# Performance work log

Measured on AMD Instinct MI355X. Metric: run time of the kernel, lower is better.

## Reference

```python
import jax, jax.numpy as jnp
import numpy as np

B, L, D, H, C = 16, 512, 1280, 512, 5


def setup_inputs() -> dict:
    key = jax.random.key(0)
    ks = jax.random.split(key, 20)
    emb = jax.random.normal(ks[0], (B, L, D), jnp.float32)
    lengths = jax.random.randint(ks[1], (B,), 16, L + 1)
    attention_mask = (jnp.arange(L)[None, :] < lengths[:, None]).astype(jnp.int32)
    sc = 1.0 / np.sqrt(H)
    u = lambda k, s: jax.random.uniform(k, s, jnp.float32, -sc, sc)
    return dict(
        embeddings=emb,
        attention_mask=attention_mask,
        h0=jax.random.normal(ks[2], (2, B, H), jnp.float32),
        c0=jax.random.normal(ks[3], (2, B, H), jnp.float32),
        w_ih_f=u(ks[4], (4 * H, D)), w_hh_f=u(ks[5], (4 * H, H)),
        b_ih_f=u(ks[6], (4 * H,)), b_hh_f=u(ks[7], (4 * H,)),
        w_ih_b=u(ks[8], (4 * H, D)), w_hh_b=u(ks[9], (4 * H, H)),
        b_ih_b=u(ks[10], (4 * H,)), b_hh_b=u(ks[11], (4 * H,)),
        w_out=u(ks[12], (2 * H, C)), b_out=u(ks[13], (C,)),
        crf_start=jax.random.normal(ks[14], (C,), jnp.float32) * 0.1,
        crf_end=jax.random.normal(ks[15], (C,), jnp.float32) * 0.1,
        crf_trans=jax.random.normal(ks[16], (C, C), jnp.float32) * 0.1,
    )


def _lstm_dir(x, h0, c0, w_ih, w_hh, b_ih, b_hh):
    # x: [B, T, D] -> hidden states [B, T, H]; PyTorch gate order (i, f, g, o)
    xg = jnp.einsum('btd,gd->btg', x, w_ih) + b_ih + b_hh  # [B, T, 4H]

    def step(carry, xw_t):
        h, c = carry
        g = xw_t + h @ w_hh.T
        i, f, gg, o = jnp.split(g, 4, axis=-1)
        c = jax.nn.sigmoid(f) * c + jax.nn.sigmoid(i) * jnp.tanh(gg)
        h = jax.nn.sigmoid(o) * jnp.tanh(c)
        return (h, c), h

    _, hs = jax.lax.scan(step, (h0, c0), xg.transpose(1, 0, 2))
    return hs.transpose(1, 0, 2)


def _emissions(embeddings, attention_mask, h0, c0, w_ih_f, w_hh_f, b_ih_f, b_hh_f,
               w_ih_b, w_hh_b, b_ih_b, b_hh_b, w_out, b_out):
    lengths = attention_mask.sum(axis=1)
    x = embeddings[:, 1:-1]                                   # drop CLS position, shift left
    Tp = x.shape[1]
    valid = jnp.arange(Tp)[None, :] < (lengths - 2)[:, None]  # remove_cls crop [1:len-1], left-aligned pad
    x = jnp.where(valid[:, :, None], x, 0.0)
    hf = _lstm_dir(x, h0[0], c0[0], w_ih_f, w_hh_f, b_ih_f, b_hh_f)
    hb = _lstm_dir(x[:, ::-1], h0[1], c0[1], w_ih_b, w_hh_b, b_ih_b, b_hh_b)[:, ::-1]
    h = jnp.concatenate([hf, hb], axis=-1)                    # [B, Tp, 2H]
    return h @ w_out + b_out, valid


def _viterbi_decode(emissions, mask, start, end, trans):
    Bn, Tp, Ct = emissions.shape
    ident = jnp.arange(Ct, dtype=jnp.int32)
    score0 = start[None, :] + emissions[:, 0]                 # [B, C]

    def step(score, inp):
        emit_t, m_t = inp                                      # [B, C], [B]
        br = score[:, :, None] + trans[None] + emit_t[:, None, :]
        ns = br.max(axis=1)
        idx = br.argmax(axis=1).astype(jnp.int32)
        idx = jnp.where(m_t[:, None], idx, ident[None, :])     # identity backpointer past seq end
        score = jnp.where(m_t[:, None], ns, score)
        return score, idx

    score, hist = jax.lax.scan(step, score0,
                               (emissions[:, 1:].transpose(1, 0, 2), mask[:, 1:].T))
    score = score + end[None, :]
    last = jnp.argmax(score, axis=-1).astype(jnp.int32)        # [B]
    bidx = jnp.arange(Bn)

    def bstep(tag, idx_t):
        prev = idx_t[bidx, tag]
        return prev, prev

    _, prevs = jax.lax.scan(bstep, last, hist, reverse=True)   # [Tp-1, B]
    tags = jnp.concatenate([prevs, last[None, :]], axis=0).transpose(1, 0)
    return tags


def reference(embeddings, attention_mask, h0, c0, w_ih_f, w_hh_f, b_ih_f, b_hh_f,
              w_ih_b, w_hh_b, b_ih_b, b_hh_b, w_out, b_out, crf_start, crf_end, crf_trans):
    emissions, valid = _emissions(embeddings, attention_mask, h0, c0,
                                  w_ih_f, w_hh_f, b_ih_f, b_hh_f,
                                  w_ih_b, w_hh_b, b_ih_b, b_hh_b, w_out, b_out)
    tags = _viterbi_decode(emissions, valid, crf_start, crf_end, crf_trans)
    return tags, valid  # tags valid where mask True (past-end entries repeat last tag)
```

## Files before the change

kernel.cpp:

```cpp
#include <hip/hip_runtime.h>

typedef unsigned short u16;
typedef unsigned int u32;
typedef __bf16 bf16x8 __attribute__((ext_vector_type(8)));
typedef u16 u16x8 __attribute__((ext_vector_type(8)));
typedef float f32x4 __attribute__((ext_vector_type(4)));

#define B_ 16
#define T_ 510
#define H_ 512
#define N_ 4096
#define KSPLIT 2560

#define OFF_ABIG  0ull
#define OFF_BBIG  41943040ull
#define OFF_BIAS  62914560ull
#define OFF_XG    62930944ull
#define OFF_HS    197148672ull
#define OFF_EMIS  230572032ull
#define OFF_V     230735232ull
#define OFF_FLAGS 230735296ull
#define OFF_HBUF  230735552ull
#define OFF_HBUFB  (OFF_EMIS)
#define OFF_FLAGSB (OFF_EMIS + 131072ull)
#define OFF_PROBE  (OFF_EMIS + 131328ull)
#define OFF_CTRL   (OFF_EMIS + 131584ull)

#define MAGIC_ 0x5EC0FFEE
#define POLL_BUDGET 65536
#define ARB_BUDGET  262144

#define GL_LDS(g, s) __builtin_amdgcn_global_load_lds(                      \
    (const __attribute__((address_space(1))) void*)(g),                     \
    (__attribute__((address_space(3))) void*)(s), 16, 0, 0)

__device__ __forceinline__ u16 f2bf(float x) {
  u32 u = __float_as_uint(x);
  u32 r = (u + 0x7fffu + ((u >> 16) & 1u)) >> 16;
  return (u16)r;
}
__device__ __forceinline__ float bf2f(u16 h) { return __uint_as_float(((u32)h) << 16); }

__device__ __forceinline__ int ld_cc(const int* p) {
  int f;
  asm volatile("global_load_dword %0, %1, off sc0 sc1\n\ts_waitcnt vmcnt(0)" : "=v"(f) : "v"(p) : "memory");
  return f;
}
__device__ __forceinline__ void st_cc(int* p, int v) {
  asm volatile("global_store_dword %0, %1, off sc0 sc1\n\ts_waitcnt vmcnt(0)" :: "v"(p), "v"(v) : "memory");
}
__device__ __forceinline__ void st_plain(int* p, int v) {
  asm volatile("global_store_dword %0, %1, off\n\ts_waitcnt vmcnt(0)" :: "v"(p), "v"(v) : "memory");
}

__global__ __launch_bounds__(256) void k_prep(const int* __restrict__ mask, int* __restrict__ V,
                                              int* __restrict__ flagsA, int* __restrict__ flagsB,
                                              int* __restrict__ probe, int* __restrict__ ctrl) {
  __shared__ int red[4];
  int b = blockIdx.x, tid = threadIdx.x;
  int s = mask[b * 512 + tid] + mask[b * 512 + 256 + tid];
  for (int off = 32; off; off >>= 1) s += __shfl_down(s, off);
  if ((tid & 63) == 0) red[tid >> 6] = s;
  __syncthreads();
  if (tid == 0) V[b] = red[0] + red[1] + red[2] + red[3] - 2;
  if (b == 0 && tid < 64) flagsA[tid] = 0;
  if (b == 2 && tid < 64) flagsB[tid] = 0;
  if (b == 3 && tid < 64) probe[tid] = 0;
  if (b == 1 && tid < 16) ctrl[tid] = 0;
}

__global__ __launch_bounds__(256) void k_valid(const int* __restrict__ V, int* __restrict__ out) {
  int idx = blockIdx.x * 256 + threadIdx.x;
  if (idx < B_ * T_) {
    int b = idx / T_, t = idx - b * T_;
    out[B_ * T_ + idx] = (t < V[b]) ? 1 : 0;
  }
}

__global__ __launch_bounds__(320) void k_splitA(const float* __restrict__ emb, const int* __restrict__ V,
                                                u16* __restrict__ Abig) {
  int row = blockIdx.x;
  int k0 = threadIdx.x * 4;
  u16* dst = Abig + (size_t)row * KSPLIT;
  float4 v = {0.f, 0.f, 0.f, 0.f};
  if (row < B_ * T_) {
    int b = row / T_, t = row - b * T_;
    if (t < V[b]) v = *(const float4*)(emb + (size_t)(b * 512 + t + 1) * 1280 + k0);
  }
  float vs[4] = {v.x, v.y, v.z, v.w};
  ushort4 hi, lo;
  u16 h0_ = f2bf(vs[0]); u16 l0_ = f2bf(vs[0] - bf2f(h0_));
  u16 h1_ = f2bf(vs[1]); u16 l1_ = f2bf(vs[1] - bf2f(h1_));
  u16 h2_ = f2bf(vs[2]); u16 l2_ = f2bf(vs[2] - bf2f(h2_));
  u16 h3_ = f2bf(vs[3]); u16 l3_ = f2bf(vs[3] - bf2f(h3_));
  hi.x = h0_; hi.y = h1_; hi.z = h2_; hi.w = h3_;
  lo.x = l0_; lo.y = l1_; lo.z = l2_; lo.w = l3_;
  *(ushort4*)(dst + k0) = hi;
  *(ushort4*)(dst + 1280 + k0) = lo;
}

__global__ __launch_bounds__(320) void k_splitB(const float* __restrict__ wf, const float* __restrict__ wb,
                                                const float* __restrict__ bihf, const float* __restrict__ bhhf,
                                                const float* __restrict__ bihb, const float* __restrict__ bhhb,
                                                u16* __restrict__ Bbig, float* __restrict__ bias) {
  int n = blockIdx.x;
  int k0 = threadIdx.x * 4;
  int d = n >> 11, g = n & 2047;
  const float* w = (d ? wb : wf) + (size_t)g * 1280;
  float4 v = *(const float4*)(w + k0);
  float vs[4] = {v.x, v.y, v.z, v.w};
  ushort4 hi, lo;
  u16 h0_ = f2bf(vs[0]); u16 l0_ = f2bf(vs[0] - bf2f(h0_));
  u16 h1_ = f2bf(vs[1]); u16 l1_ = f2bf(vs[1] - bf2f(h1_));
  u16 h2_ = f2bf(vs[2]); u16 l2_ = f2bf(vs[2] - bf2f(h2_));
  u16 h3_ = f2bf(vs[3]); u16 l3_ = f2bf(vs[3] - bf2f(h3_));
  hi.x = h0_; hi.y = h1_; hi.z = h2_; hi.w = h3_;
  lo.x = l0_; lo.y = l1_; lo.z = l2_; lo.w = l3_;
  u16* dst = Bbig + (size_t)n * KSPLIT;
  *(ushort4*)(dst + k0) = hi;
  *(ushort4*)(dst + 1280 + k0) = lo;
  if (threadIdx.x == 0) bias[n] = d ? (bihb[g] + bhhb[g]) : (bihf[g] + bhhf[g]);
}

__global__ __launch_bounds__(256, 2) void k_gemm(const u16* __restrict__ A, const u16* __restrict__ Bt,
                                                 const float* __restrict__ bias, float* __restrict__ C) {
  __shared__ __align__(16) u16 As[128 * 64];
  __shared__ __align__(16) u16 Bs[128 * 64];
  const int tid = threadIdx.x;
  const int w = tid >> 6, l = tid & 63;
  const int wm = w >> 1, wn = w & 1;
  const int bm = blockIdx.x, bn = blockIdx.y;
  f32x4 acc[4][4];
#pragma unroll
  for (int m = 0; m < 4; ++m)
#pragma unroll
    for (int n = 0; n < 4; ++n) acc[m][n] = (f32x4){0.f, 0.f, 0.f, 0.f};

  const int rQ = tid >> 3;
  const int cB = (tid & 7) * 16;
  const char* gA = (const char*)(A + (size_t)(bm * 128) * KSPLIT) + cB;
  const char* gB = (const char*)(Bt + (size_t)(bn * 128) * KSPLIT) + cB;

  for (int kt = 0; kt < 60; ++kt) {
    const int s = kt / 20, ks = kt - s * 20;
    const int aOff = ((s == 2) ? 1280 : 0) + ks * 64;
    const int bOff = ((s == 1) ? 1280 : 0) + ks * 64;
    __syncthreads();
#pragma unroll
    for (int q = 0; q < 4; ++q) {
      GL_LDS(gA + ((size_t)(q * 32 + rQ) * KSPLIT + aOff) * 2, (char*)As + q * 4096 + tid * 16);
      GL_LDS(gB + ((size_t)(q * 32 + rQ) * KSPLIT + bOff) * 2, (char*)Bs + q * 4096 + tid * 16);
    }
    __syncthreads();
#pragma unroll
    for (int kc = 0; kc < 2; ++kc) {
      bf16x8 af[4], bfr[4];
      const int kByte = kc * 64 + (l >> 4) * 16;
#pragma unroll
      for (int m = 0; m < 4; ++m)
        af[m] = *(const bf16x8*)((const char*)As + (wm * 64 + m * 16 + (l & 15)) * 128 + kByte);
#pragma unroll
      for (int n = 0; n < 4; ++n)
        bfr[n] = *(const bf16x8*)((const char*)Bs + (wn * 64 + n * 16 + (l & 15)) * 128 + kByte);
#pragma unroll
      for (int m = 0; m < 4; ++m)
#pragma unroll
        for (int n = 0; n < 4; ++n)
          acc[m][n] = __builtin_amdgcn_mfma_f32_16x16x32_bf16(af[m], bfr[n], acc[m][n], 0, 0, 0);
    }
  }
#pragma unroll
  for (int n = 0; n < 4; ++n) {
    const int gc = bn * 128 + wn * 64 + n * 16 + (l & 15);
    const float bv = bias[gc];
#pragma unroll
    for (int m = 0; m < 4; ++m) {
      const int gr0 = bm * 128 + wm * 64 + m * 16 + (l >> 4) * 4;
#pragma unroll
      for (int r = 0; r < 4; ++r) C[(size_t)(gr0 + r) * N_ + gc] = acc[m][n][r] + bv;
    }
  }
}

template <int COH>
__device__ void run_recur(int dir, int sub, const float* __restrict__ xg, const float* __restrict__ whh,
                          const float* __restrict__ h0, const float* __restrict__ c0,
                          float* __restrict__ hs, u16* __restrict__ hbuf, int* __restrict__ flags,
                          u16* lds_a, float* epil, float* hsh) {
  const int tid = threadIdx.x;
  const int w = tid >> 6, l = tid & 63;
  const int c = l & 15, kg = l >> 4;
  const int gate = c >> 2, uloc = c & 3;
  const int ug = sub * 16 + w * 4 + uloc;
  constexpr int GB = COH ? 9 : 0;

  __syncthreads();

  bf16x8 whi[16], wlo[16];
  {
    const float* wrow = whh + (size_t)(gate * 512 + ug) * 512 + kg * 8;
#pragma unroll
    for (int kc = 0; kc < 16; ++kc) {
      float4 v0 = *(const float4*)(wrow + kc * 32);
      float4 v1 = *(const float4*)(wrow + kc * 32 + 4);
      float vs[8] = {v0.x, v0.y, v0.z, v0.w, v1.x, v1.y, v1.z, v1.w};
      u16x8 hi, lo;
#pragma unroll
      for (int j = 0; j < 8; ++j) {
        u16 h = f2bf(vs[j]);
        hi[j] = h;
        lo[j] = f2bf(vs[j] - bf2f(h));
      }
      whi[kc] = __builtin_bit_cast(bf16x8, hi);
      wlo[kc] = __builtin_bit_cast(bf16x8, lo);
    }
  }

  const int eb = l & 15, eu = l >> 4;
  const int eug = sub * 16 + w * 4 + eu;
  float creg = c0[(dir * 16 + eb) * 512 + eug];
  {
    float h = h0[(dir * 16 + eb) * 512 + eug];
    u16 hh = f2bf(h), hl = f2bf(h - bf2f(hh));
    size_t base = (size_t)(dir * 2) * 8192;
    u16* p0 = hbuf + base + eb * 512 + eug;
    u16* p1 = hbuf + base + 8192 + eb * 512 + eug;
    if constexpr (COH) {
      asm volatile("global_store_short %0, %1, off\n\tglobal_store_short %2, %3, off\n\ts_waitcnt vmcnt(0)"
                   :: "v"(p0), "v"((u32)hh), "v"(p1), "v"((u32)hl) : "memory");
    } else {
      asm volatile("global_store_short %0, %1, off sc0 sc1\n\tglobal_store_short %2, %3, off sc0 sc1\n\ts_waitcnt vmcnt(0)"
                   :: "v"(p0), "v"((u32)hh), "v"(p1), "v"((u32)hl) : "memory");
    }
  }
  __syncthreads();
  if (tid == 0) {
    if constexpr (COH) st_plain(flags + dir * 32 + sub, 1 + GB);
    else st_cc(flags + dir * 32 + sub, 1 + GB);
  }

  for (int t = 0; t < T_; ++t) {
    const int trow = dir ? (T_ - 1 - t) : t;
    f32x4 acc0;
    {
      const int n = dir * 2048 + gate * 512 + ug;
#pragma unroll
      for (int r = 0; r < 4; ++r) acc0[r] = xg[(size_t)((kg * 4 + r) * T_ + trow) * N_ + n];
    }
    if (w == 0) {
      const int* fp = flags + (dir << 5) + (l & 31);
      while (true) {
        int f;
        asm volatile("global_load_dword %0, %1, off sc0 sc1\n\ts_waitcnt vmcnt(0)" : "=v"(f) : "v"(fp) : "memory");
        if (__all(f >= t + 1 + GB)) break;
        if constexpr (!COH) __builtin_amdgcn_s_sleep(1);
      }
    }
    __syncthreads();

    {
      const u16* src = hbuf + (size_t)(((t & 1) * 2 + dir) * 2) * 8192;
      uint4 v[8];
#pragma unroll
      for (int q = 0; q < 8; ++q) {
        const char* p = (const char*)src + q * 4096 + tid * 16;
        asm volatile("global_load_dwordx4 %0, %1, off sc0 sc1" : "=v"(v[q]) : "v"(p) : "memory");
      }
      asm volatile("s_waitcnt vmcnt(0)" ::: "memory");
      __builtin_amdgcn_sched_barrier(0);
#pragma unroll
      for (int q = 0; q < 8; ++q) {
        int off = q * 4096 + tid * 16;
        int var = off >> 14;
        int rem = off & 16383;
        int b = rem >> 10;
        int inrow = rem & 1023;
        *(uint4*)((char*)lds_a + var * 16384 + b * 1024 + (inrow ^ ((b & 7) << 4))) = v[q];
      }
    }
    __syncthreads();

    f32x4 acc1 = (f32x4){0.f, 0.f, 0.f, 0.f};
    f32x4 acc2 = (f32x4){0.f, 0.f, 0.f, 0.f};
    f32x4 acc3 = (f32x4){0.f, 0.f, 0.f, 0.f};
    f32x4 acc4 = (f32x4){0.f, 0.f, 0.f, 0.f};
    f32x4 acc5 = (f32x4){0.f, 0.f, 0.f, 0.f};
#pragma unroll
    for (int kc = 0; kc < 16; ++kc) {
      const int rowb = l & 15;
      const int koff = (kc * 64 + kg * 16) ^ ((rowb & 7) << 4);
      bf16x8 ahi = *(const bf16x8*)((const char*)lds_a + rowb * 1024 + koff);
      bf16x8 alo = *(const bf16x8*)((const char*)lds_a + 16384 + rowb * 1024 + koff);
      if (kc & 1) {
        acc3 = __builtin_amdgcn_mfma_f32_16x16x32_bf16(ahi, whi[kc], acc3, 0, 0, 0);
        acc4 = __builtin_amdgcn_mfma_f32_16x16x32_bf16(ahi, wlo[kc], acc4, 0, 0, 0);
        acc5 = __builtin_amdgcn_mfma_f32_16x16x32_bf16(alo, whi[kc], acc5, 0, 0, 0);
      } else {
        acc0 = __builtin_amdgcn_mfma_f32_16x16x32_bf16(ahi, whi[kc], acc0, 0, 0, 0);
        acc1 = __builtin_amdgcn_mfma_f32_16x16x32_bf16(ahi, wlo[kc], acc1, 0, 0, 0);
        acc2 = __builtin_amdgcn_mfma_f32_16x16x32_bf16(alo, whi[kc], acc2, 0, 0, 0);
      }
    }
    f32x4 acc = ((acc0 + acc3) + (acc1 + acc4)) + (acc2 + acc5);

#pragma unroll
    for (int r = 0; r < 4; ++r) epil[(w * 16 + kg * 4 + r) * 17 + c] = acc[r];
    asm volatile("s_waitcnt lgkmcnt(0)" ::: "memory");
    __builtin_amdgcn_sched_barrier(0);
    const float gi = epil[(w * 16 + eb) * 17 + 0 + eu];
    const float gf = epil[(w * 16 + eb) * 17 + 4 + eu];
    const float gg = epil[(w * 16 + eb) * 17 + 8 + eu];
    const float go = epil[(w * 16 + eb) * 17 + 12 + eu];
    const float si = 1.f / (1.f + __expf(-gi));
    const float sf = 1.f / (1.f + __expf(-gf));
    const float so = 1.f / (1.f + __expf(-go));
    const float tg = tanhf(gg);
    creg = sf * creg + si * tg;
    const float h = so * tanhf(creg);
    hsh[eb * 17 + w * 4 + eu] = h;
    __syncthreads();
    const int sb = tid >> 4, su = tid & 15;
    const float hv = hsh[sb * 17 + su];
    {
      u16 hh = f2bf(hv), hl = f2bf(hv - bf2f(hh));
      size_t base = (size_t)((((t + 1) & 1) * 2 + dir) * 2) * 8192;
      u16* p0 = hbuf + base + sb * 512 + sub * 16 + su;
      if constexpr (COH) {
        asm volatile("global_store_short %0, %1, off\n\tglobal_store_short %2, %3, off\n\ts_waitcnt vmcnt(0)"
                     :: "v"(p0), "v"((u32)hh), "v"(p0 + 8192), "v"((u32)hl) : "memory");
      } else {
        asm volatile("global_store_short %0, %1, off sc0 sc1\n\tglobal_store_short %2, %3, off sc0 sc1\n\ts_waitcnt vmcnt(0)"
                     :: "v"(p0), "v"((u32)hh), "v"(p0 + 8192), "v"((u32)hl) : "memory");
      }
    }
    __syncthreads();
    if (tid == 0) {
      if constexpr (COH) st_plain(flags + dir * 32 + sub, t + 2 + GB);
      else st_cc(flags + dir * 32 + sub, t + 2 + GB);
    }
    hs[(size_t)((dir * 16 + sb) * T_ + trow) * 512 + sub * 16 + su] = hv;
  }
}

__global__ __launch_bounds__(256, 1) void k_recur(const float* __restrict__ xg, const float* __restrict__ whh_f,
                                                  const float* __restrict__ whh_b, const float* __restrict__ h0,
                                                  const float* __restrict__ c0, float* __restrict__ hs,
                                                  u16* __restrict__ hbufA, u16* __restrict__ hbufB,
                                                  int* __restrict__ flagsA, int* __restrict__ flagsB,
                                                  int* __restrict__ probe, int* __restrict__ ctrl) {
  __shared__ __align__(16) u16 lds_a[16384];
  __shared__ float epil[4 * 16 * 17];
  __shared__ float hsh[16 * 17];
  __shared__ int s_act, s_cfg;

  const int tid = threadIdx.x;

  if (tid == 0) {
    int xcc;
    asm volatile("s_getreg_b32 %0, hwreg(HW_REG_XCC_ID)" : "=s"(xcc));
    xcc &= 7;
    int slot = 99;
    if (xcc < 2) slot = __hip_atomic_fetch_add(&ctrl[4 + xcc], 1, __ATOMIC_RELAXED, __HIP_MEMORY_SCOPE_AGENT);
    const int roleA = (xcc < 2 && slot < 32);
    const int dir = xcc, sub = slot;

    if (roleA) {
      int mg = MAGIC_;
      asm volatile("global_store_dword %0, %1, off\n\ts_waitcnt vmcnt(0)" :: "v"(probe + dir * 32 + sub), "v"(mg) : "memory");
      st_cc(flagsA + dir * 32 + sub, 2);
      bool complete = false;
      for (int it = 0; it < POLL_BUDGET && !complete; ++it) {
        complete = true;
        for (int j = 0; j < 32; ++j)
          if (ld_cc(flagsA + dir * 32 + j) < 2) { complete = false; break; }
        if (!complete) __builtin_amdgcn_s_sleep(16);
      }
      int myval = 99;
      if (complete) {
        bool ok = true;
        for (int j = 0; j < 32; ++j)
          if (ld_cc(probe + dir * 32 + j) != MAGIC_) { ok = false; break; }
        if (ok) myval = 3;
      }
      st_cc(flagsA + dir * 32 + sub, myval);
      if (sub == 0) {
        bool go = false;
        for (int it = 0; it < POLL_BUDGET; ++it) {
          int n3 = 0; bool bad = false;
          for (int j = 0; j < 32; ++j) {
            int f = ld_cc(flagsA + dir * 32 + j);
            if (f == 99) { bad = true; break; }
            if (f == 3) ++n3;
          }
          if (bad) break;
          if (n3 == 32) { go = true; break; }
          __builtin_amdgcn_s_sleep(16);
        }
        st_cc(&ctrl[12 + dir], go ? 1 : 2);
      }
    }

    if (blockIdx.x == 0) {
      int v0 = 0, v1 = 0;
      for (int it = 0; it < ARB_BUDGET; ++it) {
        v0 = ld_cc(&ctrl[12]);
        v1 = ld_cc(&ctrl[13]);
        if (v0 && v1) break;
        __builtin_amdgcn_s_sleep(16);
      }
      st_cc(&ctrl[14], 4 | (v0 == 1 ? 1 : 0) | (v1 == 1 ? 2 : 0));
    }

    int cfg;
    do {
      cfg = ld_cc(&ctrl[14]);
      if (!cfg) __builtin_amdgcn_s_sleep(16);
    } while (!cfg);

    s_cfg = cfg;
    s_act = (roleA && (cfg & (1 << dir))) ? (dir | (sub << 1)) : -1;
  }
  __syncthreads();
  const int act = s_act, cfg = s_cfg;

  if (act >= 0) {
    const int adir = act & 1, asub = act >> 1;
    run_recur<1>(adir, asub, xg, adir ? whh_b : whh_f, h0, c0, hs, hbufA, flagsA, lds_a, epil, hsh);
  }
  if (blockIdx.x < 64) {
    const int mdir = (int)blockIdx.x >> 5, msub = (int)blockIdx.x & 31;
    if (!(cfg & (1 << mdir)))
      run_recur<0>(mdir, msub, xg, mdir ? whh_b : whh_f, h0, c0, hs, hbufB, flagsB, lds_a, epil, hsh);
  }
}

__global__ __launch_bounds__(256) void k_emis(const float* __restrict__ hs, const float* __restrict__ wout,
                                              const float* __restrict__ bout, float* __restrict__ e) {
  const int tid = threadIdx.x;
  const int w = tid >> 6, l = tid & 63;
  const int row = blockIdx.x * 4 + w;
  const int b = row / T_, t = row - b * T_;
  const float* hf = hs + (size_t)(b * T_ + t) * 512;
  const float* hb = hs + (size_t)((16 + b) * T_ + t) * 512;
  float a0 = 0, a1 = 0, a2 = 0, a3 = 0, a4 = 0;
#pragma unroll
  for (int it = 0; it < 8; ++it) {
    int u = it * 64 + l;
    float hv = hf[u];
    const float* wr = wout + u * 5;
    a0 += hv * wr[0]; a1 += hv * wr[1]; a2 += hv * wr[2]; a3 += hv * wr[3]; a4 += hv * wr[4];
  }
#pragma unroll
  for (int it = 0; it < 8; ++it) {
    int u = it * 64 + l;
    float hv = hb[u];
    const float* wr = wout + (512 + u) * 5;
    a0 += hv * wr[0]; a1 += hv * wr[1]; a2 += hv * wr[2]; a3 += hv * wr[3]; a4 += hv * wr[4];
  }
  for (int off = 32; off; off >>= 1) {
    a0 += __shfl_down(a0, off);
    a1 += __shfl_down(a1, off);
    a2 += __shfl_down(a2, off);
    a3 += __shfl_down(a3, off);
    a4 += __shfl_down(a4, off);
  }
  if (l == 0) {
    float* ep = e + (size_t)row * 5;
    ep[0] = a0 + bout[0];
    ep[1] = a1 + bout[1];
    ep[2] = a2 + bout[2];
    ep[3] = a3 + bout[3];
    ep[4] = a4 + bout[4];
  }
}

__global__ __launch_bounds__(64) void k_viterbi(const float* __restrict__ e, const int* __restrict__ V,
                                                const float* __restrict__ start, const float* __restrict__ endv,
                                                const float* __restrict__ trans, int* __restrict__ out) {
  __shared__ float els[T_ * 5];
  __shared__ unsigned char hist[(T_ - 1) * 5];
  __shared__ float strans[25];
  const int b = blockIdx.x, l = threadIdx.x;
  for (int i = l; i < T_ * 5; i += 64) els[i] = e[(size_t)b * T_ * 5 + i];
  if (l < 25) strans[l] = trans[l];
  const int Vb = V[b];
  __syncthreads();
  const int cl = (l < 5) ? l : 0;
  float score = (l < 5) ? (start[l] + els[l]) : -1e30f;
  for (int t = 1; t < T_; ++t) {
    const bool valid = t < Vb;
    float m = -1e30f;
    int arg = 0;
#pragma unroll
    for (int p = 0; p < 5; ++p) {
      float v = __shfl(score, p) + strans[p * 5 + cl];
      if (v > m) { m = v; arg = p; }
    }
    if (l < 5) {
      if (valid) {
        score = m + els[t * 5 + l];
        hist[(t - 1) * 5 + l] = (unsigned char)arg;
      } else {
        hist[(t - 1) * 5 + l] = (unsigned char)l;
      }
    }
  }
  float sc = (l < 5) ? (score + endv[l]) : -1e30f;
  int last = 0;
  float mb = -1e30f;
#pragma unroll
  for (int p = 0; p < 5; ++p) {
    float v = __shfl(sc, p);
    if (v > mb) { mb = v; last = p; }
  }
  __syncthreads();
  if (l == 0) {
    int tag = last;
    out[b * T_ + (T_ - 1)] = tag;
    for (int t = T_ - 2; t >= 0; --t) {
      tag = hist[t * 5 + tag];
      out[b * T_ + t] = tag;
    }
  }
}

extern "C" void kernel_launch(void* const* d_in, const int* in_sizes, int n_in, void* d_out, int out_size,
                              void* d_ws, size_t ws_size, hipStream_t stream) {
  const float* emb = (const float*)d_in[0];
  const int* amask = (const int*)d_in[1];
  const float* h0 = (const float*)d_in[2];
  const float* c0 = (const float*)d_in[3];
  const float* wihf = (const float*)d_in[4];
  const float* whhf = (const float*)d_in[5];
  const float* bihf = (const float*)d_in[6];
  const float* bhhf = (const float*)d_in[7];
  const float* wihb = (const float*)d_in[8];
  const float* whhb = (const float*)d_in[9];
  const float* bihb = (const float*)d_in[10];
  const float* bhhb = (const float*)d_in[11];
  const float* wout = (const float*)d_in[12];
  const float* bout = (const float*)d_in[13];
  const float* cstart = (const float*)d_in[14];
  const float* cend = (const float*)d_in[15];
  const float* ctrans = (const float*)d_in[16];

  char* ws = (char*)d_ws;
  u16* Abig = (u16*)(ws + OFF_ABIG);
  u16* Bbig = (u16*)(ws + OFF_BBIG);
  float* bias = (float*)(ws + OFF_BIAS);
  float* xg = (float*)(ws + OFF_XG);
  float* hs = (float*)(ws + OFF_HS);
  float* emis = (float*)(ws + OFF_EMIS);
  int* V = (int*)(ws + OFF_V);
  int* flagsA = (int*)(ws + OFF_FLAGS);
  u16* hbufA = (u16*)(ws + OFF_HBUF);
  u16* hbufB = (u16*)(ws + OFF_HBUFB);
  int* flagsB = (int*)(ws + OFF_FLAGSB);
  int* probe = (int*)(ws + OFF_PROBE);
  int* ctrl = (int*)(ws + OFF_CTRL);
  int* out = (int*)d_out;

  hipLaunchKernelGGL(k_prep, dim3(16), dim3(256), 0, stream, amask, V, flagsA, flagsB, probe, ctrl);
  hipLaunchKernelGGL(k_valid, dim3(32), dim3(256), 0, stream, V, out);
  hipLaunchKernelGGL(k_splitA, dim3(8192), dim3(320), 0, stream, emb, V, Abig);
  hipLaunchKernelGGL(k_splitB, dim3(4096), dim3(320), 0, stream, wihf, wihb, bihf, bhhf, bihb, bhhb, Bbig, bias);
  hipLaunchKernelGGL(k_gemm, dim3(64, 32), dim3(256), 0, stream, Abig, Bbig, bias, xg);
  hipLaunchKernelGGL(k_recur, dim3(256), dim3(256), 0, stream, xg, whhf, whhb, h0, c0, hs, hbufA, hbufB,
                     flagsA, flagsB, probe, ctrl);
  hipLaunchKernelGGL(k_emis, dim3(2040), dim3(256), 0, stream, hs, wout, bout, emis);
  hipLaunchKernelGGL(k_viterbi, dim3(16), dim3(64), 0, stream, emis, V, cstart, cend, ctrans, out);
}
```

Before: 1.775 ms.

## Replace per-step flag polling with generation-tagged hidden-state chunks in LSTM recurrence

The recurrent kernel no longer publishes h through a separate buffer plus a per-block flag. Each block now writes 16-byte chunks that carry the bf16 hi/lo h values together with a generation counter, and consumers spin on the chunk tags directly. This removes the flag store/poll round trip and a barrier from every serial timestep. It also issues the xg input loads early so they overlap the wait, and replaces tanhf/division with exp+rcp approximations. The chunk buffers are placed at workspace offset 0 (the Abig region), which depends on Abig being dead by then, and rcp-based activations are slightly less accurate.

```diff
diff --git a/kernel.cpp b/kernel.cpp
--- a/kernel.cpp
+++ b/kernel.cpp
@@ -5,6 +5,8 @@
 typedef __bf16 bf16x8 __attribute__((ext_vector_type(8)));
 typedef u16 u16x8 __attribute__((ext_vector_type(8)));
 typedef float f32x4 __attribute__((ext_vector_type(4)));
+typedef u32 u32x2 __attribute__((ext_vector_type(2)));
+typedef u32 u32x4 __attribute__((ext_vector_type(4)));
 
 #define B_ 16
 #define T_ 510
@@ -20,11 +22,10 @@
 #define OFF_EMIS  230572032ull
 #define OFF_V     230735232ull
 #define OFF_FLAGS 230735296ull
-#define OFF_HBUF  230735552ull
-#define OFF_HBUFB  (OFF_EMIS)
-#define OFF_FLAGSB (OFF_EMIS + 131072ull)
 #define OFF_PROBE  (OFF_EMIS + 131328ull)
 #define OFF_CTRL   (OFF_EMIS + 131584ull)
+#define CHUNKA_OFF 0ull
+#define CHUNKB_OFF 262144ull
 
 #define MAGIC_ 0x5EC0FFEE
 #define POLL_BUDGET 65536
@@ -49,13 +50,19 @@
 __device__ __forceinline__ void st_cc(int* p, int v) {
   asm volatile("global_store_dword %0, %1, off sc0 sc1\n\ts_waitcnt vmcnt(0)" :: "v"(p), "v"(v) : "memory");
 }
-__device__ __forceinline__ void st_plain(int* p, int v) {
-  asm volatile("global_store_dword %0, %1, off\n\ts_waitcnt vmcnt(0)" :: "v"(p), "v"(v) : "memory");
+
+__device__ __forceinline__ float sigm_f(float x) {
+  float e = __expf(-x);
+  return __builtin_amdgcn_rcpf(1.f + e);
+}
+__device__ __forceinline__ float tanh_f(float x) {
+  float e = __expf(2.f * x);
+  return 1.f - 2.f * __builtin_amdgcn_rcpf(e + 1.f);
 }
 
 __global__ __launch_bounds__(256) void k_prep(const int* __restrict__ mask, int* __restrict__ V,
-                                              int* __restrict__ flagsA, int* __restrict__ flagsB,
-                                              int* __restrict__ probe, int* __restrict__ ctrl) {
+                                              int* __restrict__ flagsA, int* __restrict__ probe,
+                                              int* __restrict__ ctrl) {
   __shared__ int red[4];
   int b = blockIdx.x, tid = threadIdx.x;
   int s = mask[b * 512 + tid] + mask[b * 512 + 256 + tid];
@@ -64,9 +71,14 @@
   __syncthreads();
   if (tid == 0) V[b] = red[0] + red[1] + red[2] + red[3] - 2;
   if (b == 0 && tid < 64) flagsA[tid] = 0;
-  if (b == 2 && tid < 64) flagsB[tid] = 0;
   if (b == 3 && tid < 64) probe[tid] = 0;
   if (b == 1 && tid < 16) ctrl[tid] = 0;
+}
+
+__global__ __launch_bounds__(256) void k_zero(char* __restrict__ p) {
+  u32x4 z = (u32x4){0u, 0u, 0u, 0u};
+  char* dst = p + ((size_t)blockIdx.x * 256 + threadIdx.x) * 16;
+  asm volatile("global_store_dwordx4 %0, %1, off sc0 sc1" :: "v"(dst), "v"(z) : "memory");
 }
 
 __global__ __launch_bounds__(256) void k_valid(const int* __restrict__ V, int* __restrict__ out) {
@@ -183,16 +195,31 @@
 }
 
 template <int COH>
+__device__ __forceinline__ void emit_chunks(char* buf, int sub, u32 gen, const u16* pack) {
+  const int tid = threadIdx.x;
+  if (tid < 128) {
+    const int sb = tid >> 3, r = tid & 7, p = r >> 2, j = r & 3;
+    const u32* pw = (const u32*)(pack + p * 256 + sb * 16 + j * 4);
+    u32x4 val;
+    val[0] = pw[0]; val[1] = pw[1]; val[2] = gen; val[3] = 0u;
+    char* dst = buf + sb * 4096 + p * 2048 + (sub * 4 + j) * 16;
+    if constexpr (COH)
+      asm volatile("global_store_dwordx4 %0, %1, off" :: "v"(dst), "v"(val) : "memory");
+    else
+      asm volatile("global_store_dwordx4 %0, %1, off sc0 sc1" :: "v"(dst), "v"(val) : "memory");
+  }
+}
+
+template <int COH>
 __device__ void run_recur(int dir, int sub, const float* __restrict__ xg, const float* __restrict__ whh,
                           const float* __restrict__ h0, const float* __restrict__ c0,
-                          float* __restrict__ hs, u16* __restrict__ hbuf, int* __restrict__ flags,
-                          u16* lds_a, float* epil, float* hsh) {
+                          float* __restrict__ hs, char* __restrict__ cb,
+                          u16* lds_a, float* epil, u16* pack) {
   const int tid = threadIdx.x;
   const int w = tid >> 6, l = tid & 63;
   const int c = l & 15, kg = l >> 4;
   const int gate = c >> 2, uloc = c & 3;
   const int ug = sub * 16 + w * 4 + uloc;
-  constexpr int GB = COH ? 9 : 0;
 
   __syncthreads();
 
@@ -216,75 +243,61 @@
     }
   }
 
-  const int eb = l & 15, eu = l >> 4;
-  const int eug = sub * 16 + w * 4 + eu;
-  float creg = c0[(dir * 16 + eb) * 512 + eug];
+  const int sb = tid >> 4, su = tid & 15;
+  const int gu = sub * 16 + su;
+  float creg = c0[(dir * 16 + sb) * 512 + gu];
   {
-    float h = h0[(dir * 16 + eb) * 512 + eug];
+    float h = h0[(dir * 16 + sb) * 512 + gu];
     u16 hh = f2bf(h), hl = f2bf(h - bf2f(hh));
-    size_t base = (size_t)(dir * 2) * 8192;
-    u16* p0 = hbuf + base + eb * 512 + eug;
-    u16* p1 = hbuf + base + 8192 + eb * 512 + eug;
-    if constexpr (COH) {
-      asm volatile("global_store_short %0, %1, off\n\tglobal_store_short %2, %3, off\n\ts_waitcnt vmcnt(0)"
-                   :: "v"(p0), "v"((u32)hh), "v"(p1), "v"((u32)hl) : "memory");
-    } else {
-      asm volatile("global_store_short %0, %1, off sc0 sc1\n\tglobal_store_short %2, %3, off sc0 sc1\n\ts_waitcnt vmcnt(0)"
-                   :: "v"(p0), "v"((u32)hh), "v"(p1), "v"((u32)hl) : "memory");
-    }
+    pack[sb * 16 + su] = hh;
+    pack[256 + sb * 16 + su] = hl;
   }
   __syncthreads();
-  if (tid == 0) {
-    if constexpr (COH) st_plain(flags + dir * 32 + sub, 1 + GB);
-    else st_cc(flags + dir * 32 + sub, 1 + GB);
-  }
+  emit_chunks<COH>(cb + 65536, sub, 1u, pack);
 
   for (int t = 0; t < T_; ++t) {
     const int trow = dir ? (T_ - 1 - t) : t;
-    f32x4 acc0;
-    {
-      const int n = dir * 2048 + gate * 512 + ug;
-#pragma unroll
-      for (int r = 0; r < 4; ++r) acc0[r] = xg[(size_t)((kg * 4 + r) * T_ + trow) * N_ + n];
-    }
-    if (w == 0) {
-      const int* fp = flags + (dir << 5) + (l & 31);
-      while (true) {
-        int f;
-        asm volatile("global_load_dword %0, %1, off sc0 sc1\n\ts_waitcnt vmcnt(0)" : "=v"(f) : "v"(fp) : "memory");
-        if (__all(f >= t + 1 + GB)) break;
-        if constexpr (!COH) __builtin_amdgcn_s_sleep(1);
-      }
-    }
-    __syncthreads();
-
-    {
-      const u16* src = hbuf + (size_t)(((t & 1) * 2 + dir) * 2) * 8192;
-      uint4 v[8];
-#pragma unroll
-      for (int q = 0; q < 8; ++q) {
-        const char* p = (const char*)src + q * 4096 + tid * 16;
-        asm volatile("global_load_dwordx4 %0, %1, off sc0 sc1" : "=v"(v[q]) : "v"(p) : "memory");
-      }
+    const u32 gen = (u32)(t + 1);
+    const char* sbuf = cb + ((t + 1) & 1) * 65536;
+
+    u32x4 v[16];
+#pragma unroll
+    for (int i = 0; i < 16; ++i) {
+      const char* p = sbuf + ((size_t)(tid + 256 * i)) * 16;
+      asm volatile("global_load_dwordx4 %0, %1, off sc0 sc1" : "=v"(v[i]) : "v"(p) : "memory");
+    }
+    float xv[4];
+#pragma unroll
+    for (int g = 0; g < 4; ++g) {
+      const float* p = xg + (size_t)(sb * T_ + trow) * N_ + dir * 2048 + g * 512 + gu;
+      asm volatile("global_load_dword %0, %1, off" : "=v"(xv[g]) : "v"(p) : "memory");
+    }
+    asm volatile("s_waitcnt vmcnt(4)" ::: "memory");
+    __builtin_amdgcn_sched_barrier(0);
+    while (true) {
+      u32 bad = 0;
+#pragma unroll
+      for (int i = 0; i < 16; ++i) bad |= (v[i][2] != gen) ? (1u << i) : 0u;
+      if (!bad) break;
+#pragma unroll
+      for (int i = 0; i < 16; ++i)
+        if (bad & (1u << i)) {
+          const char* p = sbuf + ((size_t)(tid + 256 * i)) * 16;
+          asm volatile("global_load_dwordx4 %0, %1, off sc0 sc1" : "=v"(v[i]) : "v"(p) : "memory");
+        }
       asm volatile("s_waitcnt vmcnt(0)" ::: "memory");
       __builtin_amdgcn_sched_barrier(0);
-#pragma unroll
-      for (int q = 0; q < 8; ++q) {
-        int off = q * 4096 + tid * 16;
-        int var = off >> 14;
-        int rem = off & 16383;
-        int b = rem >> 10;
-        int inrow = rem & 1023;
-        *(uint4*)((char*)lds_a + var * 16384 + b * 1024 + (inrow ^ ((b & 7) << 4))) = v[q];
-      }
+    }
+#pragma unroll
+    for (int i = 0; i < 16; ++i) {
+      int ci = tid + 256 * i;
+      int b = ci >> 8, pl = (ci >> 7) & 1, k = ci & 127;
+      int off = pl * 16384 + b * 1024 + ((k * 8) ^ ((b & 7) << 4));
+      *(u32x2*)((char*)lds_a + off) = (u32x2){v[i][0], v[i][1]};
     }
     __syncthreads();
 
-    f32x4 acc1 = (f32x4){0.f, 0.f, 0.f, 0.f};
-    f32x4 acc2 = (f32x4){0.f, 0.f, 0.f, 0.f};
-    f32x4 acc3 = (f32x4){0.f, 0.f, 0.f, 0.f};
-    f32x4 acc4 = (f32x4){0.f, 0.f, 0.f, 0.f};
-    f32x4 acc5 = (f32x4){0.f, 0.f, 0.f, 0.f};
+    f32x4 a0 = (f32x4){0.f, 0.f, 0.f, 0.f}, a1 = a0, a2 = a0, a3 = a0, a4 = a0, a5 = a0;
 #pragma unroll
     for (int kc = 0; kc < 16; ++kc) {
       const int rowb = l & 15;
@@ -292,65 +305,53 @@
       bf16x8 ahi = *(const bf16x8*)((const char*)lds_a + rowb * 1024 + koff);
       bf16x8 alo = *(const bf16x8*)((const char*)lds_a + 16384 + rowb * 1024 + koff);
       if (kc & 1) {
-        acc3 = __builtin_amdgcn_mfma_f32_16x16x32_bf16(ahi, whi[kc], acc3, 0, 0, 0);
-        acc4 = __builtin_amdgcn_mfma_f32_16x16x32_bf16(ahi, wlo[kc], acc4, 0, 0, 0);
-        acc5 = __builtin_amdgcn_mfma_f32_16x16x32_bf16(alo, whi[kc], acc5, 0, 0, 0);
+        a3 = __builtin_amdgcn_mfma_f32_16x16x32_bf16(ahi, whi[kc], a3, 0, 0, 0);
+        a4 = __builtin_amdgcn_mfma_f32_16x16x32_bf16(ahi, wlo[kc], a4, 0, 0, 0);
+        a5 = __builtin_amdgcn_mfma_f32_16x16x32_bf16(alo, whi[kc], a5, 0, 0, 0);
       } else {
-        acc0 = __builtin_amdgcn_mfma_f32_16x16x32_bf16(ahi, whi[kc], acc0, 0, 0, 0);
-        acc1 = __builtin_amdgcn_mfma_f32_16x16x32_bf16(ahi, wlo[kc], acc1, 0, 0, 0);
-        acc2 = __builtin_amdgcn_mfma_f32_16x16x32_bf16(alo, whi[kc], acc2, 0, 0, 0);
-      }
-    }
-    f32x4 acc = ((acc0 + acc3) + (acc1 + acc4)) + (acc2 + acc5);
-
-#pragma unroll
-    for (int r = 0; r < 4; ++r) epil[(w * 16 + kg * 4 + r) * 17 + c] = acc[r];
-    asm volatile("s_waitcnt lgkmcnt(0)" ::: "memory");
+        a0 = __builtin_amdgcn_mfma_f32_16x16x32_bf16(ahi, whi[kc], a0, 0, 0, 0);
+        a1 = __builtin_amdgcn_mfma_f32_16x16x32_bf16(ahi, wlo[kc], a1, 0, 0, 0);
+        a2 = __builtin_amdgcn_mfma_f32_16x16x32_bf16(alo, whi[kc], a2, 0, 0, 0);
+      }
+    }
+    f32x4 acc = ((a0 + a3) + (a1 + a4)) + (a2 + a5);
+
+#pragma unroll
+    for (int r = 0; r < 4; ++r) epil[w * 280 + (kg * 4 + r) * 17 + c] = acc[r];
+    __syncthreads();
+    asm volatile("s_waitcnt vmcnt(0)" ::: "memory");
     __builtin_amdgcn_sched_barrier(0);
-    const float gi = epil[(w * 16 + eb) * 17 + 0 + eu];
-    const float gf = epil[(w * 16 + eb) * 17 + 4 + eu];
-    const float gg = epil[(w * 16 + eb) * 17 + 8 + eu];
-    const float go = epil[(w * 16 + eb) * 17 + 12 + eu];
-    const float si = 1.f / (1.f + __expf(-gi));
-    const float sf = 1.f / (1.f + __expf(-gf));
-    const float so = 1.f / (1.f + __expf(-go));
-    const float tg = tanhf(gg);
+    const int ew = su >> 2, ec = su & 3;
+    const float gi = epil[ew * 280 + sb * 17 + 0 + ec] + xv[0];
+    const float gf = epil[ew * 280 + sb * 17 + 4 + ec] + xv[1];
+    const float gg = epil[ew * 280 + sb * 17 + 8 + ec] + xv[2];
+    const float go = epil[ew * 280 + sb * 17 + 12 + ec] + xv[3];
+    const float si = sigm_f(gi);
+    const float sf = sigm_f(gf);
+    const float so = sigm_f(go);
+    const float tg = tanh_f(gg);
     creg = sf * creg + si * tg;
-    const float h = so * tanhf(creg);
-    hsh[eb * 17 + w * 4 + eu] = h;
+    const float h = so * tanh_f(creg);
+    {
+      u16 hh = f2bf(h), hl = f2bf(h - bf2f(hh));
+      pack[sb * 16 + su] = hh;
+      pack[256 + sb * 16 + su] = hl;
+    }
     __syncthreads();
-    const int sb = tid >> 4, su = tid & 15;
-    const float hv = hsh[sb * 17 + su];
-    {
-      u16 hh = f2bf(hv), hl = f2bf(hv - bf2f(hh));
-      size_t base = (size_t)((((t + 1) & 1) * 2 + dir) * 2) * 8192;
-      u16* p0 = hbuf + base + sb * 512 + sub * 16 + su;
-      if constexpr (COH) {
-        asm volatile("global_store_short %0, %1, off\n\tglobal_store_short %2, %3, off\n\ts_waitcnt vmcnt(0)"
-                     :: "v"(p0), "v"((u32)hh), "v"(p0 + 8192), "v"((u32)hl) : "memory");
-      } else {
-        asm volatile("global_store_short %0, %1, off sc0 sc1\n\tglobal_store_short %2, %3, off sc0 sc1\n\ts_waitcnt vmcnt(0)"
-                     :: "v"(p0), "v"((u32)hh), "v"(p0 + 8192), "v"((u32)hl) : "memory");
-      }
-    }
-    __syncthreads();
-    if (tid == 0) {
-      if constexpr (COH) st_plain(flags + dir * 32 + sub, t + 2 + GB);
-      else st_cc(flags + dir * 32 + sub, t + 2 + GB);
-    }
-    hs[(size_t)((dir * 16 + sb) * T_ + trow) * 512 + sub * 16 + su] = hv;
+    emit_chunks<COH>(cb + (t & 1) * 65536, sub, (u32)(t + 2), pack);
+    hs[(size_t)((dir * 16 + sb) * T_ + trow) * 512 + gu] = h;
   }
 }
 
 __global__ __launch_bounds__(256, 1) void k_recur(const float* __restrict__ xg, const float* __restrict__ whh_f,
                                                   const float* __restrict__ whh_b, const float* __restrict__ h0,
                                                   const float* __restrict__ c0, float* __restrict__ hs,
-                                                  u16* __restrict__ hbufA, u16* __restrict__ hbufB,
-                                                  int* __restrict__ flagsA, int* __restrict__ flagsB,
-                                                  int* __restrict__ probe, int* __restrict__ ctrl) {
+                                                  char* __restrict__ chunkA, char* __restrict__ chunkB,
+                                                  int* __restrict__ flagsA, int* __restrict__ probe,
+                                                  int* __restrict__ ctrl) {
   __shared__ __align__(16) u16 lds_a[16384];
-  __shared__ float epil[4 * 16 * 17];
-  __shared__ float hsh[16 * 17];
+  __shared__ float epil[4 * 280];
+  __shared__ u16 pack[512];
   __shared__ int s_act, s_cfg;
 
   const int tid = threadIdx.x;
@@ -425,12 +426,14 @@
 
   if (act >= 0) {
     const int adir = act & 1, asub = act >> 1;
-    run_recur<1>(adir, asub, xg, adir ? whh_b : whh_f, h0, c0, hs, hbufA, flagsA, lds_a, epil, hsh);
+    run_recur<1>(adir, asub, xg, adir ? whh_b : whh_f, h0, c0, hs,
+                 chunkA + adir * 131072, lds_a, epil, pack);
   }
   if (blockIdx.x < 64) {
     const int mdir = (int)blockIdx.x >> 5, msub = (int)blockIdx.x & 31;
     if (!(cfg & (1 << mdir)))
-      run_recur<0>(mdir, msub, xg, mdir ? whh_b : whh_f, h0, c0, hs, hbufB, flagsB, lds_a, epil, hsh);
+      run_recur<0>(mdir, msub, xg, mdir ? whh_b : whh_f, h0, c0, hs,
+                   chunkB + mdir * 131072, lds_a, epil, pack);
   }
 }
 
@@ -553,20 +556,20 @@
   float* emis = (float*)(ws + OFF_EMIS);
   int* V = (int*)(ws + OFF_V);
   int* flagsA = (int*)(ws + OFF_FLAGS);
-  u16* hbufA = (u16*)(ws + OFF_HBUF);
-  u16* hbufB = (u16*)(ws + OFF_HBUFB);
-  int* flagsB = (int*)(ws + OFF_FLAGSB);
   int* probe = (int*)(ws + OFF_PROBE);
   int* ctrl = (int*)(ws + OFF_CTRL);
+  char* chunkA = ws + CHUNKA_OFF;
+  char* chunkB = ws + CHUNKB_OFF;
   int* out = (int*)d_out;
 
-  hipLaunchKernelGGL(k_prep, dim3(16), dim3(256), 0, stream, amask, V, flagsA, flagsB, probe, ctrl);
+  hipLaunchKernelGGL(k_prep, dim3(16), dim3(256), 0, stream, amask, V, flagsA, probe, ctrl);
   hipLaunchKernelGGL(k_valid, dim3(32), dim3(256), 0, stream, V, out);
   hipLaunchKernelGGL(k_splitA, dim3(8192), dim3(320), 0, stream, emb, V, Abig);
   hipLaunchKernelGGL(k_splitB, dim3(4096), dim3(320), 0, stream, wihf, wihb, bihf, bhhf, bihb, bhhb, Bbig, bias);
   hipLaunchKernelGGL(k_gemm, dim3(64, 32), dim3(256), 0, stream, Abig, Bbig, bias, xg);
-  hipLaunchKernelGGL(k_recur, dim3(256), dim3(256), 0, stream, xg, whhf, whhb, h0, c0, hs, hbufA, hbufB,
-                     flagsA, flagsB, probe, ctrl);
+  hipLaunchKernelGGL(k_zero, dim3(128), dim3(256), 0, stream, chunkA);
+  hipLaunchKernelGGL(k_recur, dim3(256), dim3(256), 0, stream, xg, whhf, whhb, h0, c0, hs,
+                     chunkA, chunkB, flagsA, probe, ctrl);
   hipLaunchKernelGGL(k_emis, dim3(2040), dim3(256), 0, stream, hs, wout, bout, emis);
   hipLaunchKernelGGL(k_viterbi, dim3(16), dim3(64), 0, stream, emis, V, cstart, cend, ctrans, out);
 }
```

Result: slower. 1.826 ms (+2.9%).

## Add runtime probe to use sc0-only loads for same-XCC recurrence handshakes

Applied to the files above, without the earlier changes.

Extends the startup handshake among the 32 blocks of each direction. If they can verify that stores are seen through the shared L2 using loads without the sc1 system-coherence bit, they switch to a third recurrence mode. In that mode flag polling and h-buffer loads use sc0 only, with an occasional full-coherence flag load as a fallback. The aim is to cut the latency of the per-timestep cross-block synchronisation. The cost is a longer multi-phase handshake at startup and a risk of stale reads if the probe's verdict is wrong.

```diff
diff --git a/kernel.cpp b/kernel.cpp
--- a/kernel.cpp
+++ b/kernel.cpp
@@ -5,6 +5,7 @@
 typedef __bf16 bf16x8 __attribute__((ext_vector_type(8)));
 typedef u16 u16x8 __attribute__((ext_vector_type(8)));
 typedef float f32x4 __attribute__((ext_vector_type(4)));
+typedef u32 u32x4 __attribute__((ext_vector_type(4)));
 
 #define B_ 16
 #define T_ 510
@@ -25,9 +26,13 @@
 #define OFF_FLAGSB (OFF_EMIS + 131072ull)
 #define OFF_PROBE  (OFF_EMIS + 131328ull)
 #define OFF_CTRL   (OFF_EMIS + 131584ull)
-
-#define MAGIC_ 0x5EC0FFEE
+#define OFF_PROBE2 (OFF_EMIS + 131648ull)
+
+#define MAGIC_  0x5EC0FFEE
+#define MAGIC2_ 0x7A57C0DE
+#define MAGIC3_ 0x3C0DE777
 #define POLL_BUDGET 65536
+#define PHB_BUDGET  8192
 #define ARB_BUDGET  262144
 
 #define GL_LDS(g, s) __builtin_amdgcn_global_load_lds(                      \
@@ -46,6 +51,11 @@
   asm volatile("global_load_dword %0, %1, off sc0 sc1\n\ts_waitcnt vmcnt(0)" : "=v"(f) : "v"(p) : "memory");
   return f;
 }
+__device__ __forceinline__ int ld_se(const int* p) {
+  int f;
+  asm volatile("global_load_dword %0, %1, off sc0\n\ts_waitcnt vmcnt(0)" : "=v"(f) : "v"(p) : "memory");
+  return f;
+}
 __device__ __forceinline__ void st_cc(int* p, int v) {
   asm volatile("global_store_dword %0, %1, off sc0 sc1\n\ts_waitcnt vmcnt(0)" :: "v"(p), "v"(v) : "memory");
 }
@@ -55,7 +65,8 @@
 
 __global__ __launch_bounds__(256) void k_prep(const int* __restrict__ mask, int* __restrict__ V,
                                               int* __restrict__ flagsA, int* __restrict__ flagsB,
-                                              int* __restrict__ probe, int* __restrict__ ctrl) {
+                                              int* __restrict__ probe, int* __restrict__ probe2,
+                                              int* __restrict__ ctrl) {
   __shared__ int red[4];
   int b = blockIdx.x, tid = threadIdx.x;
   int s = mask[b * 512 + tid] + mask[b * 512 + 256 + tid];
@@ -66,6 +77,7 @@
   if (b == 0 && tid < 64) flagsA[tid] = 0;
   if (b == 2 && tid < 64) flagsB[tid] = 0;
   if (b == 3 && tid < 64) probe[tid] = 0;
+  if (b == 4 && tid < 64) probe2[tid] = 0;
   if (b == 1 && tid < 16) ctrl[tid] = 0;
 }
 
@@ -192,7 +204,7 @@
   const int c = l & 15, kg = l >> 4;
   const int gate = c >> 2, uloc = c & 3;
   const int ug = sub * 16 + w * 4 + uloc;
-  constexpr int GB = COH ? 9 : 0;
+  constexpr int GB = (COH != 0) ? 9 : 0;
 
   __syncthreads();
 
@@ -225,7 +237,7 @@
     size_t base = (size_t)(dir * 2) * 8192;
     u16* p0 = hbuf + base + eb * 512 + eug;
     u16* p1 = hbuf + base + 8192 + eb * 512 + eug;
-    if constexpr (COH) {
+    if constexpr (COH != 0) {
       asm volatile("global_store_short %0, %1, off\n\tglobal_store_short %2, %3, off\n\ts_waitcnt vmcnt(0)"
                    :: "v"(p0), "v"((u32)hh), "v"(p1), "v"((u32)hl) : "memory");
     } else {
@@ -235,7 +247,7 @@
   }
   __syncthreads();
   if (tid == 0) {
-    if constexpr (COH) st_plain(flags + dir * 32 + sub, 1 + GB);
+    if constexpr (COH != 0) st_plain(flags + dir * 32 + sub, 1 + GB);
     else st_cc(flags + dir * 32 + sub, 1 + GB);
   }
 
@@ -249,22 +261,34 @@
     }
     if (w == 0) {
       const int* fp = flags + (dir << 5) + (l & 31);
+      int it = 0;
       while (true) {
         int f;
-        asm volatile("global_load_dword %0, %1, off sc0 sc1\n\ts_waitcnt vmcnt(0)" : "=v"(f) : "v"(fp) : "memory");
+        if constexpr (COH == 2) {
+          ++it;
+          if ((it & 255) == 0)
+            asm volatile("global_load_dword %0, %1, off sc0 sc1\n\ts_waitcnt vmcnt(0)" : "=v"(f) : "v"(fp) : "memory");
+          else
+            asm volatile("global_load_dword %0, %1, off sc0\n\ts_waitcnt vmcnt(0)" : "=v"(f) : "v"(fp) : "memory");
+        } else {
+          asm volatile("global_load_dword %0, %1, off sc0 sc1\n\ts_waitcnt vmcnt(0)" : "=v"(f) : "v"(fp) : "memory");
+        }
         if (__all(f >= t + 1 + GB)) break;
-        if constexpr (!COH) __builtin_amdgcn_s_sleep(1);
+        if constexpr (COH == 0) __builtin_amdgcn_s_sleep(1);
       }
     }
     __syncthreads();
 
     {
       const u16* src = hbuf + (size_t)(((t & 1) * 2 + dir) * 2) * 8192;
-      uint4 v[8];
+      u32x4 v[8];
 #pragma unroll
       for (int q = 0; q < 8; ++q) {
         const char* p = (const char*)src + q * 4096 + tid * 16;
-        asm volatile("global_load_dwordx4 %0, %1, off sc0 sc1" : "=v"(v[q]) : "v"(p) : "memory");
+        if constexpr (COH == 2)
+          asm volatile("global_load_dwordx4 %0, %1, off sc0" : "=v"(v[q]) : "v"(p) : "memory");
+        else
+          asm volatile("global_load_dwordx4 %0, %1, off sc0 sc1" : "=v"(v[q]) : "v"(p) : "memory");
       }
       asm volatile("s_waitcnt vmcnt(0)" ::: "memory");
       __builtin_amdgcn_sched_barrier(0);
@@ -275,7 +299,7 @@
         int rem = off & 16383;
         int b = rem >> 10;
         int inrow = rem & 1023;
-        *(uint4*)((char*)lds_a + var * 16384 + b * 1024 + (inrow ^ ((b & 7) << 4))) = v[q];
+        *(u32x4*)((char*)lds_a + var * 16384 + b * 1024 + (inrow ^ ((b & 7) << 4))) = v[q];
       }
     }
     __syncthreads();
@@ -325,7 +349,7 @@
       u16 hh = f2bf(hv), hl = f2bf(hv - bf2f(hh));
       size_t base = (size_t)((((t + 1) & 1) * 2 + dir) * 2) * 8192;
       u16* p0 = hbuf + base + sb * 512 + sub * 16 + su;
-      if constexpr (COH) {
+      if constexpr (COH != 0) {
         asm volatile("global_store_short %0, %1, off\n\tglobal_store_short %2, %3, off\n\ts_waitcnt vmcnt(0)"
                      :: "v"(p0), "v"((u32)hh), "v"(p0 + 8192), "v"((u32)hl) : "memory");
       } else {
@@ -335,7 +359,7 @@
     }
     __syncthreads();
     if (tid == 0) {
-      if constexpr (COH) st_plain(flags + dir * 32 + sub, t + 2 + GB);
+      if constexpr (COH != 0) st_plain(flags + dir * 32 + sub, t + 2 + GB);
       else st_cc(flags + dir * 32 + sub, t + 2 + GB);
     }
     hs[(size_t)((dir * 16 + sb) * T_ + trow) * 512 + sub * 16 + su] = hv;
@@ -347,7 +371,8 @@
                                                   const float* __restrict__ c0, float* __restrict__ hs,
                                                   u16* __restrict__ hbufA, u16* __restrict__ hbufB,
                                                   int* __restrict__ flagsA, int* __restrict__ flagsB,
-                                                  int* __restrict__ probe, int* __restrict__ ctrl) {
+                                                  int* __restrict__ probe, int* __restrict__ probe2,
+                                                  int* __restrict__ ctrl) {
   __shared__ __align__(16) u16 lds_a[16384];
   __shared__ float epil[4 * 16 * 17];
   __shared__ float hsh[16 * 17];
@@ -363,40 +388,91 @@
     if (xcc < 2) slot = __hip_atomic_fetch_add(&ctrl[4 + xcc], 1, __ATOMIC_RELAXED, __HIP_MEMORY_SCOPE_AGENT);
     const int roleA = (xcc < 2 && slot < 32);
     const int dir = xcc, sub = slot;
-
     if (roleA) {
+      int* myflag = flagsA + dir * 32 + sub;
+      const int fb = dir * 32;
       int mg = MAGIC_;
-      asm volatile("global_store_dword %0, %1, off\n\ts_waitcnt vmcnt(0)" :: "v"(probe + dir * 32 + sub), "v"(mg) : "memory");
-      st_cc(flagsA + dir * 32 + sub, 2);
+      asm volatile("global_store_dword %0, %1, off\n\ts_waitcnt vmcnt(0)" :: "v"(probe + fb + sub), "v"(mg) : "memory");
+      st_cc(myflag, 2);
       bool complete = false;
       for (int it = 0; it < POLL_BUDGET && !complete; ++it) {
         complete = true;
         for (int j = 0; j < 32; ++j)
-          if (ld_cc(flagsA + dir * 32 + j) < 2) { complete = false; break; }
+          if (ld_cc(flagsA + fb + j) < 2) { complete = false; break; }
         if (!complete) __builtin_amdgcn_s_sleep(16);
       }
-      int myval = 99;
-      if (complete) {
-        bool ok = true;
+      bool Aok = complete;
+      if (Aok)
         for (int j = 0; j < 32; ++j)
-          if (ld_cc(probe + dir * 32 + j) != MAGIC_) { ok = false; break; }
-        if (ok) myval = 3;
-      }
-      st_cc(flagsA + dir * 32 + sub, myval);
+          if (ld_cc(probe + fb + j) != MAGIC_) { Aok = false; break; }
+      if (Aok) {
+        int m2 = MAGIC2_;
+        asm volatile("global_store_dword %0, %1, off\n\ts_waitcnt vmcnt(0)" :: "v"(probe2 + fb + sub), "v"(m2) : "memory");
+      }
+      st_cc(myflag, Aok ? 3 : 7);
+      bool any7 = !Aok, arrived = false;
+      for (int it = 0; it < PHB_BUDGET && !arrived && !any7; ++it) {
+        arrived = true;
+        for (int j = 0; j < 32; ++j) {
+          int f = ld_cc(flagsA + fb + j);
+          if (f == 7) { any7 = true; break; }
+          if (f < 3) { arrived = false; break; }
+        }
+        if (!arrived && !any7) __builtin_amdgcn_s_sleep(4);
+      }
+      if (Aok && arrived && !any7) {
+        bool r1 = true;
+        for (int j = 0; j < 32; ++j)
+          if (ld_se(probe2 + fb + j) != MAGIC2_) { r1 = false; break; }
+        st_cc(myflag, r1 ? 4 : 8);
+        if (r1) {
+          bool all4 = false, any8 = false;
+          for (int it = 0; it < PHB_BUDGET && !all4 && !any8; ++it) {
+            all4 = true;
+            for (int j = 0; j < 32; ++j) {
+              int f = ld_cc(flagsA + fb + j);
+              if (f == 8) { any8 = true; break; }
+              if (f < 4) { all4 = false; break; }
+            }
+            if (!all4 && !any8) __builtin_amdgcn_s_sleep(4);
+          }
+          if (all4 && !any8) {
+            int m3 = MAGIC3_;
+            asm volatile("global_store_dword %0, %1, off\n\ts_waitcnt vmcnt(0)" :: "v"(probe2 + fb + sub), "v"(m3) : "memory");
+            st_cc(myflag, 5);
+            bool all5 = false;
+            for (int it = 0; it < PHB_BUDGET && !all5; ++it) {
+              all5 = true;
+              for (int j = 0; j < 32; ++j)
+                if (ld_cc(flagsA + fb + j) < 5) { all5 = false; break; }
+              if (!all5) __builtin_amdgcn_s_sleep(4);
+            }
+            bool r2 = all5;
+            if (r2)
+              for (int j = 0; j < 32; ++j)
+                if (ld_se(probe2 + fb + j) != MAGIC3_) { r2 = false; break; }
+            st_cc(myflag, r2 ? 6 : 8);
+          }
+        }
+      }
       if (sub == 0) {
-        bool go = false;
-        for (int it = 0; it < POLL_BUDGET; ++it) {
-          int n3 = 0; bool bad = false;
+        int verdict = Aok ? 1 : 2;
+        for (int it = 0; it < PHB_BUDGET; ++it) {
+          int n6 = 0;
+          bool bad7 = false, bad8 = false, pending = false;
           for (int j = 0; j < 32; ++j) {
-            int f = ld_cc(flagsA + dir * 32 + j);
-            if (f == 99) { bad = true; break; }
-            if (f == 3) ++n3;
+            int f = ld_cc(flagsA + fb + j);
+            if (f == 7) { bad7 = true; break; }
+            if (f == 8) { bad8 = true; break; }
+            if (f == 6) ++n6;
+            else pending = true;
           }
-          if (bad) break;
-          if (n3 == 32) { go = true; break; }
-          __builtin_amdgcn_s_sleep(16);
+          if (bad7) { verdict = 2; break; }
+          if (bad8) { verdict = Aok ? 1 : 2; break; }
+          if (n6 == 32) { verdict = 3; break; }
+          if (pending) __builtin_amdgcn_s_sleep(4);
         }
-        st_cc(&ctrl[12 + dir], go ? 1 : 2);
+        st_cc(&ctrl[12 + dir], verdict);
       }
     }
 
@@ -408,7 +484,9 @@
         if (v0 && v1) break;
         __builtin_amdgcn_s_sleep(16);
       }
-      st_cc(&ctrl[14], 4 | (v0 == 1 ? 1 : 0) | (v1 == 1 ? 2 : 0));
+      if (!v0) v0 = 2;
+      if (!v1) v1 = 2;
+      st_cc(&ctrl[14], 0x100 | v0 | (v1 << 4));
     }
 
     int cfg;
@@ -418,18 +496,22 @@
     } while (!cfg);
 
     s_cfg = cfg;
-    s_act = (roleA && (cfg & (1 << dir))) ? (dir | (sub << 1)) : -1;
+    int md = (cfg >> (dir * 4)) & 15;
+    s_act = (roleA && md != 2) ? (dir | (sub << 1) | (md << 6)) : -1;
   }
   __syncthreads();
   const int act = s_act, cfg = s_cfg;
 
   if (act >= 0) {
-    const int adir = act & 1, asub = act >> 1;
-    run_recur<1>(adir, asub, xg, adir ? whh_b : whh_f, h0, c0, hs, hbufA, flagsA, lds_a, epil, hsh);
+    const int adir = act & 1, asub = (act >> 1) & 31, md = act >> 6;
+    if (md == 3)
+      run_recur<2>(adir, asub, xg, adir ? whh_b : whh_f, h0, c0, hs, hbufA, flagsA, lds_a, epil, hsh);
+    else
+      run_recur<1>(adir, asub, xg, adir ? whh_b : whh_f, h0, c0, hs, hbufA, flagsA, lds_a, epil, hsh);
   }
   if (blockIdx.x < 64) {
     const int mdir = (int)blockIdx.x >> 5, msub = (int)blockIdx.x & 31;
-    if (!(cfg & (1 << mdir)))
+    if (((cfg >> (mdir * 4)) & 15) == 2)
       run_recur<0>(mdir, msub, xg, mdir ? whh_b : whh_f, h0, c0, hs, hbufB, flagsB, lds_a, epil, hsh);
   }
 }
@@ -557,16 +639,17 @@
   u16* hbufB = (u16*)(ws + OFF_HBUFB);
   int* flagsB = (int*)(ws + OFF_FLAGSB);
   int* probe = (int*)(ws + OFF_PROBE);
+  int* probe2 = (int*)(ws + OFF_PROBE2);
   int* ctrl = (int*)(ws + OFF_CTRL);
   int* out = (int*)d_out;
 
-  hipLaunchKernelGGL(k_prep, dim3(16), dim3(256), 0, stream, amask, V, flagsA, flagsB, probe, ctrl);
+  hipLaunchKernelGGL(k_prep, dim3(16), dim3(256), 0, stream, amask, V, flagsA, flagsB, probe, probe2, ctrl);
   hipLaunchKernelGGL(k_valid, dim3(32), dim3(256), 0, stream, V, out);
   hipLaunchKernelGGL(k_splitA, dim3(8192), dim3(320), 0, stream, emb, V, Abig);
   hipLaunchKernelGGL(k_splitB, dim3(4096), dim3(320), 0, stream, wihf, wihb, bihf, bhhf, bihb, bhhb, Bbig, bias);
   hipLaunchKernelGGL(k_gemm, dim3(64, 32), dim3(256), 0, stream, Abig, Bbig, bias, xg);
   hipLaunchKernelGGL(k_recur, dim3(256), dim3(256), 0, stream, xg, whhf, whhb, h0, c0, hs, hbufA, hbufB,
-                     flagsA, flagsB, probe, ctrl);
+                     flagsA, flagsB, probe, probe2, ctrl);
   hipLaunchKernelGGL(k_emis, dim3(2040), dim3(256), 0, stream, hs, wout, bout, emis);
   hipLaunchKernelGGL(k_viterbi, dim3(16), dim3(64), 0, stream, emis, V, cstart, cend, ctrans, out);
 }
```

Result: faster. 1.634 ms (-7.9%).
